# Performance work log

Hardware: AMD Instinct MI355X
Metric: run time of the kernel (lower is better)

The kernel has to match this reference:

```python
import jax, jax.numpy as jnp
import numpy as np

START_TIME = 10
CODING_TIME = 10
REMAIN_TIME = 5
V_TH = 1.0

# surrogate-gradient spike: forward is Heaviside(x>0)
@jax.custom_vjp
def spike(x):
    return (x > 0).astype(x.dtype)

def _spike_fwd(x):
    return spike(x), x

def _spike_bwd(x, g):
    lens = 0.5
    gamma = 0.5
    temp = jnp.exp(-x * x / (2.0 * lens * lens)) / jnp.sqrt(2.0 * jnp.pi) / lens
    return (g * temp * gamma,)

spike.defvjp(_spike_fwd, _spike_bwd)

B, T, I, H, O = 500, 100, 700, 512, 20

def setup_inputs() -> dict:
    key = jax.random.key(0)
    ks = jax.random.split(key, 9)
    half = I // 2
    input_data = jax.random.normal(ks[0], (B, T, I), dtype=jnp.float32)
    target = jax.random.randint(ks[1], (B, T), 0, O, dtype=jnp.int32).astype(jnp.int64)
    v_init = jax.random.uniform(ks[2], (B, H), dtype=jnp.float32)  # torch.rand init
    lim = 1.0 / np.sqrt(half)
    W1 = jax.random.uniform(ks[3], (H, half), minval=-lim, maxval=lim, dtype=jnp.float32)
    W2 = jax.random.uniform(ks[4], (H, half), minval=-lim, maxval=lim, dtype=jnp.float32)
    tau_n = jax.random.uniform(ks[5], (2, H), minval=2.0, maxval=6.0, dtype=jnp.float32)
    tau_m = jax.random.uniform(ks[6], (H,), minval=0.0, maxval=4.0, dtype=jnp.float32)
    lim_o = 1.0 / np.sqrt(H)
    Wout = jax.random.uniform(ks[7], (O, H), minval=-lim_o, maxval=lim_o, dtype=jnp.float32)
    bout = jax.random.uniform(ks[8], (O,), minval=-lim_o, maxval=lim_o, dtype=jnp.float32)
    return {"input_data": input_data, "target": target, "v_init": v_init,
            "W1": W1, "W2": W2, "tau_n": tau_n, "tau_m": tau_m,
            "Wout": Wout, "bout": bout}

def reference(input_data, target, v_init, W1, W2, tau_n, tau_m, Wout, bout):
    Bs, Ts, Is = input_data.shape
    half = Is // 2
    # precompute both branch drives for all timesteps: [T, B, H]
    b1 = jnp.einsum('bti,hi->tbh', input_data[:, :, :half], W1)
    b2 = jnp.einsum('bti,hi->tbh', input_data[:, :, half:], W2)
    beta1 = jax.nn.sigmoid(tau_n[0])  # [H]
    beta2 = jax.nn.sigmoid(tau_n[1])  # [H]
    alpha = jax.nn.sigmoid(tau_m)     # [H]

    def step(carry, inp):
        d1, d2, v, s = carry
        x1, x2 = inp
        d1 = beta1 * d1 + (1.0 - beta1) * x1
        d2 = beta2 * d2 + (1.0 - beta2) * x2
        v = alpha * v + (1.0 - alpha) * (d1 + d2) - V_TH * s
        s = spike(v - V_TH)
        return (d1, d2, v, s), s

    z = jnp.zeros_like(v_init)
    (_, _, _, _), spikes = jax.lax.scan(step, (z, z, v_init, z), (b1, b2))  # spikes: [T,B,H]
    output_history = jnp.einsum('tbh,oh->bto', spikes, Wout) + bout  # [B,T,O]

    ts = np.arange(Ts)
    mask_np = ((ts - START_TIME) % (CODING_TIME + REMAIN_TIME) > REMAIN_TIME) & (ts > START_TIME)
    mask = jnp.asarray(mask_np, dtype=output_history.dtype)  # [T]

    # faithful double-softmax: CrossEntropyLoss applied to softmax(output)
    p = jax.nn.softmax(output_history, axis=-1)
    logp = jax.nn.log_softmax(p, axis=-1)
    tgt = target.astype(jnp.int32)
    ce = -jnp.take_along_axis(logp, tgt[..., None], axis=-1)[..., 0]  # [B,T]
    loss_per_t = ce.mean(axis=0)  # mean over batch, per timestep
    total_loss = jnp.sum(loss_per_t * mask)

    pred = jnp.argmax(p, axis=-1)  # [B,T]
    total_correct = jnp.sum((pred == tgt).astype(jnp.int32) * mask_np[None, :].astype(np.int32))
    total_samples = int(mask_np.sum()) * Bs
    return total_loss, output_history, total_correct, total_samples
```

## Files before the change

kernel.cpp:

```cpp
#include <hip/hip_runtime.h>
#include <hip/hip_bf16.h>
#include <math.h>

#define B_    500
#define T_    100
#define I_    700
#define HALF_ 350
#define H_    512
#define O_    20
#define M_    (B_*T_)
#define BH_   (B_*H_)
#define TP_   112
#define KP_   352
#define ASTR_ 40
#define ABUF_ (TP_*ASTR_)
#define DRB_  116
#define NB_   12500

#define START_T  10
#define CODING_T 10
#define REMAIN_T 5

typedef __attribute__((ext_vector_type(8))) short short8v;
typedef __attribute__((ext_vector_type(8))) unsigned short ushort8v;
typedef __attribute__((ext_vector_type(4))) float f32x4;
typedef __attribute__((ext_vector_type(2))) float f32x2;

__device__ __forceinline__ float sigmoidf_(float x) {
  return 1.0f / (1.0f + expf(-x));
}

__device__ __forceinline__ unsigned cvtpk(float lo, float hi) {
  unsigned r;
  asm("v_cvt_pk_bf16_f32 %0, %1, %2" : "=v"(r) : "v"(lo), "v"(hi));
  return r;
}

__device__ __forceinline__ unsigned cvtpk_fp8x4(float f0, float f1, float f2, float f3) {
  int r = __builtin_amdgcn_cvt_pk_fp8_f32(f0, f1, 0, false);
  r = __builtin_amdgcn_cvt_pk_fp8_f32(f2, f3, r, true);
  return (unsigned)r;
}

__device__ __forceinline__ unsigned short f2bf(float f) {
  unsigned u = __float_as_uint(f);
  u = (u + 0x7fffu + ((u >> 16) & 1u)) >> 16;
  return (unsigned short)u;
}

__global__ __launch_bounds__(256) void convert_w(
    const float* __restrict__ W1, const float* __restrict__ W2,
    unsigned short* __restrict__ wb)
{
  const int idx = blockIdx.x * 256 + threadIdx.x;
  const int ph  = idx / (H_ * (KP_ / 8));
  const int rem = idx % (H_ * (KP_ / 8));
  const int h   = rem / (KP_ / 8);
  const int cc  = (rem % (KP_ / 8)) * 8;
  ushort8v v;
#pragma unroll
  for (int j = 0; j < 8; ++j) {
    const int kk = cc + j;
    float f;
    if (ph == 0) f = (kk < HALF_) ? W1[(size_t)h * HALF_ + kk] : 0.0f;
    else         f = (kk >= 2)    ? W2[(size_t)h * HALF_ + kk - 2] : 0.0f;
    v[j] = f2bf(f);
  }
  *reinterpret_cast<ushort8v*>(wb + (((size_t)ph * H_ + h) * KP_) + cc) = v;
}

__global__ __launch_bounds__(1024, 4) void fused_drive_scan(
    const float* __restrict__ input, const unsigned short* __restrict__ Wb,
    const float* __restrict__ v_init, const float* __restrict__ tau_n,
    const float* __restrict__ tau_m, unsigned char* __restrict__ spikes)
{
  __shared__ __align__(16) unsigned short As[2 * ABUF_];
  __shared__ __align__(4) unsigned char d1c[H_ * DRB_];
  __shared__ __align__(4) unsigned char d2c[H_ * DRB_];

  const int tid  = threadIdx.x;
  const int lane = tid & 63;
  const int w    = tid >> 6;
  const int b    = blockIdx.x;

  const int sr = tid >> 3;
  const int so = (tid & 7) * 4;
  const bool stLd = (tid < 800);
  const bool stZr = (tid >= 800) && (tid < 896);
  const float* aBase = input + ((size_t)b * T_ + (stLd ? sr : 0)) * I_ + so;
  unsigned short* aDst = As + sr * ASTR_ + so;

  const int brow = w * 32 + (lane & 15);
  const int kcS  = (lane >> 4) * 8;
  const unsigned short* bBase0 = Wb + (size_t)brow * KP_ + kcS;
  const unsigned short* bBase1 = Wb + (size_t)(brow + 16) * KP_ + kcS;
  const int arow = lane & 15;

  f32x4 acc[7][2];
#pragma unroll
  for (int i = 0; i < 7; ++i) {
    acc[i][0] = f32x4{0.f, 0.f, 0.f, 0.f};
    acc[i][1] = f32x4{0.f, 0.f, 0.f, 0.f};
  }

  float4 aR;
  short8v bC0, bC1, bN0, bN1;

  if (stZr) {
    const uint2 z = {0, 0};
    *(uint2*)(aDst) = z;
    *(uint2*)(aDst + ABUF_) = z;
  }
  if (stLd) aR = *(const float4*)(aBase);
  bC0 = *reinterpret_cast<const short8v*>(bBase0);
  bC1 = *reinterpret_cast<const short8v*>(bBase1);
  bN0 = *reinterpret_cast<const short8v*>(bBase0 + 32);
  bN1 = *reinterpret_cast<const short8v*>(bBase1 + 32);
  if (stLd) {
    const uint2 p = {cvtpk(aR.x, aR.y), cvtpk(aR.z, aR.w)};
    *(uint2*)(aDst) = p;
    aR = *(const float4*)(aBase + 32);
  }
  asm volatile("s_waitcnt lgkmcnt(0)" ::: "memory");
  __builtin_amdgcn_s_barrier();
  asm volatile("" ::: "memory");

#pragma unroll 1
  for (int k = 0; k < 22; ++k) {
    const int buf  = (k & 1) * ABUF_;
    const int nbuf = ((k + 1) & 1) * ABUF_;
    short8v a[7];
#pragma unroll
    for (int i = 0; i < 7; ++i)
      a[i] = *reinterpret_cast<const short8v*>(As + buf + (arow + i * 16) * ASTR_ + kcS);
#pragma unroll
    for (int i = 0; i < 7; ++i) {
      acc[i][0] = __builtin_amdgcn_mfma_f32_16x16x32_bf16(a[i], bC0, acc[i][0], 0, 0, 0);
      acc[i][1] = __builtin_amdgcn_mfma_f32_16x16x32_bf16(a[i], bC1, acc[i][1], 0, 0, 0);
    }
    bC0 = bN0; bC1 = bN1;
    if (k < 21 && stLd) {
      const uint2 p = {cvtpk(aR.x, aR.y), cvtpk(aR.z, aR.w)};
      *(uint2*)(aDst + nbuf) = p;
    }
    if (k < 20 && stLd) {
      const int kn  = k + 2;
      const int ph  = (kn >= 11);
      const int k0  = (kn - ph * 11) * 32;
      aR = *(const float4*)(aBase + (ph ? 348 : 0) + k0);
    }
    if (k < 20) {
      const int kb  = k + 2;
      const int phb = (kb >= 11);
      const size_t bo = (size_t)phb * H_ * KP_ + (kb - phb * 11) * 32;
      bN0 = *reinterpret_cast<const short8v*>(bBase0 + bo);
      bN1 = *reinterpret_cast<const short8v*>(bBase1 + bo);
    }
    if (k == 10 || k == 21) {
      unsigned char* ds = (k == 10) ? d1c : d2c;
#pragma unroll
      for (int i = 0; i < 7; ++i) {
        const int tb = i * 16 + ((lane >> 4) << 2);
#pragma unroll
        for (int j = 0; j < 2; ++j) {
          const int hl = w * 32 + j * 16 + (lane & 15);
          const unsigned r =
              cvtpk_fp8x4(acc[i][j][0], acc[i][j][1], acc[i][j][2], acc[i][j][3]);
          *(unsigned*)(ds + hl * DRB_ + tb) = r;
          acc[i][j] = f32x4{0.f, 0.f, 0.f, 0.f};
        }
      }
    }
    asm volatile("s_waitcnt lgkmcnt(0)" ::: "memory");
    __builtin_amdgcn_s_barrier();
    asm volatile("" ::: "memory");
  }

  if (tid < H_) {
    const int hg = tid;
    const float beta1 = sigmoidf_(tau_n[hg]);
    const float beta2 = sigmoidf_(tau_n[H_ + hg]);
    const float alpha = sigmoidf_(tau_m[hg]);
    const float ob1 = 1.0f - beta1, ob2 = 1.0f - beta2, oa = 1.0f - alpha;

    float d1 = 0.0f, d2 = 0.0f, s = 0.0f;
    float v = v_init[(size_t)b * H_ + hg];
    const unsigned char* r1 = d1c + hg * DRB_;
    const unsigned char* r2 = d2c + hg * DRB_;
    unsigned char* sp = spikes + (size_t)b * (T_ * H_) + hg;
#pragma unroll 1
    for (int c = 0; c < 25; ++c) {
      const unsigned u1 = *(const unsigned*)(r1 + c * 4);
      const unsigned u2 = *(const unsigned*)(r2 + c * 4);
      const f32x2 a1 = __builtin_amdgcn_cvt_pk_f32_fp8((int)u1, false);
      const f32x2 b1 = __builtin_amdgcn_cvt_pk_f32_fp8((int)u1, true);
      const f32x2 a2 = __builtin_amdgcn_cvt_pk_f32_fp8((int)u2, false);
      const f32x2 b2 = __builtin_amdgcn_cvt_pk_f32_fp8((int)u2, true);
      const float f1[4] = {a1[0], a1[1], b1[0], b1[1]};
      const float f2[4] = {a2[0], a2[1], b2[0], b2[1]};
#pragma unroll
      for (int j = 0; j < 4; ++j) {
        d1 = beta1 * d1 + ob1 * f1[j];
        d2 = beta2 * d2 + ob2 * f2[j];
        v = alpha * v + oa * (d1 + d2) - s;
        s = (v > 1.0f) ? 1.0f : 0.0f;
        sp[(size_t)(c * 4 + j) * H_] = (unsigned char)s;
      }
    }
  }
}

__global__ __launch_bounds__(256) void out_loss(
    const unsigned char* __restrict__ spikes, const float* __restrict__ Wout,
    const float* __restrict__ bout, const int* __restrict__ target,
    float* __restrict__ oh, float* __restrict__ partials)
{
  const int lane = threadIdx.x & 63;
  const int widx = threadIdx.x >> 6;
  const int bt = blockIdx.x * 4 + widx;
  const int t = bt % T_;

  const uint2 sv = *(const uint2*)(spikes + (size_t)bt * H_ + lane * 8);

  float acc[O_];
#pragma unroll
  for (int o = 0; o < O_; ++o) acc[o] = 0.0f;

#pragma unroll
  for (int j = 0; j < 8; ++j) {
    const unsigned sb = ((j < 4) ? (sv.x >> (8 * j)) : (sv.y >> (8 * (j - 4)))) & 255u;
    if (sb) {
      const int hh = lane * 8 + j;
#pragma unroll
      for (int o = 0; o < O_; ++o) acc[o] += Wout[o * H_ + hh];
    }
  }
#pragma unroll
  for (int o = 0; o < O_; ++o) {
#pragma unroll
    for (int off = 32; off; off >>= 1) acc[o] += __shfl_xor(acc[o], off);
    acc[o] += bout[o];
  }
  if (lane < O_) oh[(size_t)bt * O_ + lane] = acc[lane];

  __shared__ float sl[4], sc[4];
  float lossc = 0.0f, corr = 0.0f;
  const bool maskv = (t > START_T) && (((t - START_T) % (CODING_T + REMAIN_T)) > REMAIN_T);
  if (maskv) {
    const int tgt = target[bt];
    float m = acc[0];
    int pred = 0;
#pragma unroll
    for (int o = 1; o < O_; ++o) { if (acc[o] > m) { m = acc[o]; pred = o; } }
    float S = 0.0f, etgt = 0.0f;
#pragma unroll
    for (int o = 0; o < O_; ++o) {
      const float eo = expf(acc[o] - m);
      S += eo;
      if (o == tgt) etgt = eo;
    }
    const float inv = 1.0f / S;
    float S2 = 0.0f;
#pragma unroll
    for (int o = 0; o < O_; ++o) S2 += expf(expf(acc[o] - m) * inv - inv);
    lossc = (inv + logf(S2) - etgt * inv) * (1.0f / (float)B_);
    corr = (pred == tgt) ? 1.0f : 0.0f;
  }
  if (lane == 0) { sl[widx] = lossc; sc[widx] = corr; }
  __syncthreads();
  if (threadIdx.x == 0) {
    partials[blockIdx.x]       = sl[0] + sl[1] + sl[2] + sl[3];
    partials[NB_ + blockIdx.x] = sc[0] + sc[1] + sc[2] + sc[3];
  }
}

__global__ __launch_bounds__(256) void loss_final(
    const float* __restrict__ partials, float* __restrict__ out, float samples)
{
  float a = 0.0f, c = 0.0f;
  for (int i = threadIdx.x; i < NB_; i += 256) { a += partials[i]; c += partials[NB_ + i]; }
  __shared__ float sl[256], sc[256];
  sl[threadIdx.x] = a; sc[threadIdx.x] = c;
  __syncthreads();
  for (int s = 128; s > 0; s >>= 1) {
    if (threadIdx.x < s) {
      sl[threadIdx.x] += sl[threadIdx.x + s];
      sc[threadIdx.x] += sc[threadIdx.x + s];
    }
    __syncthreads();
  }
  if (threadIdx.x == 0) {
    out[0] = sl[0];
    out[1 + (size_t)M_ * O_] = sc[0];
    out[2 + (size_t)M_ * O_] = samples;
  }
}

extern "C" void kernel_launch(void* const* d_in, const int* in_sizes, int n_in,
                              void* d_out, int out_size, void* d_ws, size_t ws_size,
                              hipStream_t stream) {
  const float* input  = (const float*)d_in[0];
  const int*   target = (const int*)d_in[1];
  const float* v_init = (const float*)d_in[2];
  const float* W1     = (const float*)d_in[3];
  const float* W2     = (const float*)d_in[4];
  const float* tau_n  = (const float*)d_in[5];
  const float* tau_m  = (const float*)d_in[6];
  const float* Wout   = (const float*)d_in[7];
  const float* bout   = (const float*)d_in[8];
  float* out = (float*)d_out;
  float* oh  = out + 1;

  unsigned short* Wb = (unsigned short*)d_ws;
  unsigned char* spikes = (unsigned char*)(Wb + (size_t)2 * H_ * KP_);
  float* partials = (float*)(spikes + (size_t)B_ * T_ * H_);

  hipLaunchKernelGGL(convert_w, dim3((2 * H_ * KP_ / 8) / 256), dim3(256), 0, stream,
                     W1, W2, Wb);

  hipLaunchKernelGGL(fused_drive_scan, dim3(B_), dim3(1024), 0, stream,
                     input, Wb, v_init, tau_n, tau_m, spikes);

  hipLaunchKernelGGL(out_loss, dim3(NB_), dim3(256), 0, stream,
                     spikes, Wout, bout, target, oh, partials);

  int mcount = 0;
  for (int t = 0; t < T_; ++t)
    if (t > START_T && ((t - START_T) % (CODING_T + REMAIN_T)) > REMAIN_T) mcount++;
  hipLaunchKernelGGL(loss_final, dim3(1), dim3(256), 0, stream, partials,
                     out, (float)(mcount * B_));
}
```

Before: 162.6 us.

## Split fused drive-scan across two blocks per batch row by hidden half

Each batch element's drive GEMM and scan is now handled by two 512-thread blocks, each covering 256 hidden units, instead of one 1024-thread block covering all 512. This doubles the grid to 1000 blocks and halves the per-block LDS used for the fp8 drive buffers, which should let more blocks share a CU and improve occupancy and load balance. The A-tile staging is widened so each thread converts 8 floats per step. The cost is that each batch row's input slice is loaded and converted twice, once per hidden half.

```diff
diff --git a/kernel.cpp b/kernel.cpp
--- a/kernel.cpp
+++ b/kernel.cpp
@@ -14,6 +14,7 @@
 #define KP_   352
 #define ASTR_ 40
 #define ABUF_ (TP_*ASTR_)
+#define HH_   256
 #define DRB_  116
 #define NB_   12500
 
@@ -69,28 +70,31 @@
   *reinterpret_cast<ushort8v*>(wb + (((size_t)ph * H_ + h) * KP_) + cc) = v;
 }
 
-__global__ __launch_bounds__(1024, 4) void fused_drive_scan(
+__global__ __launch_bounds__(512, 4) void fused_drive_scan(
     const float* __restrict__ input, const unsigned short* __restrict__ Wb,
     const float* __restrict__ v_init, const float* __restrict__ tau_n,
     const float* __restrict__ tau_m, unsigned char* __restrict__ spikes)
 {
   __shared__ __align__(16) unsigned short As[2 * ABUF_];
-  __shared__ __align__(4) unsigned char d1c[H_ * DRB_];
-  __shared__ __align__(4) unsigned char d2c[H_ * DRB_];
+  __shared__ __align__(4) unsigned char d1c[HH_ * DRB_];
+  __shared__ __align__(4) unsigned char d2c[HH_ * DRB_];
 
   const int tid  = threadIdx.x;
   const int lane = tid & 63;
   const int w    = tid >> 6;
-  const int b    = blockIdx.x;
-
-  const int sr = tid >> 3;
-  const int so = (tid & 7) * 4;
-  const bool stLd = (tid < 800);
-  const bool stZr = (tid >= 800) && (tid < 896);
-  const float* aBase = input + ((size_t)b * T_ + (stLd ? sr : 0)) * I_ + so;
-  unsigned short* aDst = As + sr * ASTR_ + so;
-
-  const int brow = w * 32 + (lane & 15);
+  const int id   = blockIdx.x;
+  const int b    = id >> 1;
+  const int hh   = id & 1;
+  const int h0g  = hh * HH_;
+
+  const int sr = tid >> 2;
+  const int sc = (tid & 3) * 8;
+  const bool stLd = (sr < T_);
+  const bool stZr = (sr >= T_) && (sr < TP_);
+  const float* aBase = input + ((size_t)b * T_ + (stLd ? sr : 0)) * I_ + sc;
+  unsigned short* aDst = As + sr * ASTR_ + sc;
+
+  const int brow = h0g + w * 32 + (lane & 15);
   const int kcS  = (lane >> 4) * 8;
   const unsigned short* bBase0 = Wb + (size_t)brow * KP_ + kcS;
   const unsigned short* bBase1 = Wb + (size_t)(brow + 16) * KP_ + kcS;
@@ -103,23 +107,28 @@
     acc[i][1] = f32x4{0.f, 0.f, 0.f, 0.f};
   }
 
-  float4 aR;
+  float4 aR0, aR1;
   short8v bC0, bC1, bN0, bN1;
 
   if (stZr) {
-    const uint2 z = {0, 0};
-    *(uint2*)(aDst) = z;
-    *(uint2*)(aDst + ABUF_) = z;
-  }
-  if (stLd) aR = *(const float4*)(aBase);
+    const uint4 z = {0, 0, 0, 0};
+    *(uint4*)(aDst) = z;
+    *(uint4*)(aDst + ABUF_) = z;
+  }
+  if (stLd) {
+    aR0 = *(const float4*)(aBase);
+    aR1 = *(const float4*)(aBase + 4);
+  }
   bC0 = *reinterpret_cast<const short8v*>(bBase0);
   bC1 = *reinterpret_cast<const short8v*>(bBase1);
   bN0 = *reinterpret_cast<const short8v*>(bBase0 + 32);
   bN1 = *reinterpret_cast<const short8v*>(bBase1 + 32);
   if (stLd) {
-    const uint2 p = {cvtpk(aR.x, aR.y), cvtpk(aR.z, aR.w)};
-    *(uint2*)(aDst) = p;
-    aR = *(const float4*)(aBase + 32);
+    const uint4 p = {cvtpk(aR0.x, aR0.y), cvtpk(aR0.z, aR0.w),
+                     cvtpk(aR1.x, aR1.y), cvtpk(aR1.z, aR1.w)};
+    *(uint4*)(aDst) = p;
+    aR0 = *(const float4*)(aBase + 32);
+    aR1 = *(const float4*)(aBase + 36);
   }
   asm volatile("s_waitcnt lgkmcnt(0)" ::: "memory");
   __builtin_amdgcn_s_barrier();
@@ -140,14 +149,17 @@
     }
     bC0 = bN0; bC1 = bN1;
     if (k < 21 && stLd) {
-      const uint2 p = {cvtpk(aR.x, aR.y), cvtpk(aR.z, aR.w)};
-      *(uint2*)(aDst + nbuf) = p;
+      const uint4 p = {cvtpk(aR0.x, aR0.y), cvtpk(aR0.z, aR0.w),
+                       cvtpk(aR1.x, aR1.y), cvtpk(aR1.z, aR1.w)};
+      *(uint4*)(aDst + nbuf) = p;
     }
     if (k < 20 && stLd) {
       const int kn  = k + 2;
       const int ph  = (kn >= 11);
       const int k0  = (kn - ph * 11) * 32;
-      aR = *(const float4*)(aBase + (ph ? 348 : 0) + k0);
+      const float* ap = aBase + (ph ? 348 : 0) + k0;
+      aR0 = *(const float4*)(ap);
+      aR1 = *(const float4*)(ap + 4);
     }
     if (k < 20) {
       const int kb  = k + 2;
@@ -176,8 +188,8 @@
     asm volatile("" ::: "memory");
   }
 
-  if (tid < H_) {
-    const int hg = tid;
+  if (tid < HH_) {
+    const int hg = h0g + tid;
     const float beta1 = sigmoidf_(tau_n[hg]);
     const float beta2 = sigmoidf_(tau_n[H_ + hg]);
     const float alpha = sigmoidf_(tau_m[hg]);
@@ -185,8 +197,8 @@
 
     float d1 = 0.0f, d2 = 0.0f, s = 0.0f;
     float v = v_init[(size_t)b * H_ + hg];
-    const unsigned char* r1 = d1c + hg * DRB_;
-    const unsigned char* r2 = d2c + hg * DRB_;
+    const unsigned char* r1 = d1c + tid * DRB_;
+    const unsigned char* r2 = d2c + tid * DRB_;
     unsigned char* sp = spikes + (size_t)b * (T_ * H_) + hg;
 #pragma unroll 1
     for (int c = 0; c < 25; ++c) {
@@ -318,7 +330,7 @@
   hipLaunchKernelGGL(convert_w, dim3((2 * H_ * KP_ / 8) / 256), dim3(256), 0, stream,
                      W1, W2, Wb);
 
-  hipLaunchKernelGGL(fused_drive_scan, dim3(B_), dim3(1024), 0, stream,
+  hipLaunchKernelGGL(fused_drive_scan, dim3(2 * B_), dim3(512), 0, stream,
                      input, Wb, v_init, tau_n, tau_m, spikes);
 
   hipLaunchKernelGGL(out_loss, dim3(NB_), dim3(256), 0, stream,
```

Measured after the change: 165.1 us. No clear change (+1.5%).

## Load input tiles directly into LDS as fp32 and convert to bf16 on fragment read

Applied to the files above, without the earlier changes.

Input rows now go straight from global memory into a double-buffered fp32 LDS tile through global_load_lds, replacing the old path of staging in registers, converting, and storing bf16 into LDS. Each wave converts fp32 to bf16 when it reads its MFMA A fragments, and the loop syncs on vmcnt instead of lgkmcnt. The aim is to drop the register staging step and its latency from the GEMM prologue and loop. In exchange, LDS read traffic doubles and every wave repeats the same conversion work. Padded rows past T now load row 0 data instead of zeros.

```diff
diff --git a/kernel.cpp b/kernel.cpp
--- a/kernel.cpp
+++ b/kernel.cpp
@@ -12,8 +12,7 @@
 #define BH_   (B_*H_)
 #define TP_   112
 #define KP_   352
-#define ASTR_ 40
-#define ABUF_ (TP_*ASTR_)
+#define AFP_  3584
 #define DRB_  116
 #define NB_   12500
 
@@ -46,6 +45,12 @@
   unsigned u = __float_as_uint(f);
   u = (u + 0x7fffu + ((u >> 16) & 1u)) >> 16;
   return (unsigned short)u;
+}
+
+__device__ __forceinline__ void gload16f(const float* g, float* l) {
+  __builtin_amdgcn_global_load_lds(
+      (const __attribute__((address_space(1))) unsigned int*)g,
+      (__attribute__((address_space(3))) unsigned int*)l, 16, 0, 0);
 }
 
 __global__ __launch_bounds__(256) void convert_w(
@@ -74,7 +79,7 @@
     const float* __restrict__ v_init, const float* __restrict__ tau_n,
     const float* __restrict__ tau_m, unsigned char* __restrict__ spikes)
 {
-  __shared__ __align__(16) unsigned short As[2 * ABUF_];
+  __shared__ __align__(16) float Af[2 * AFP_];
   __shared__ __align__(4) unsigned char d1c[H_ * DRB_];
   __shared__ __align__(4) unsigned char d2c[H_ * DRB_];
 
@@ -83,18 +88,18 @@
   const int w    = tid >> 6;
   const int b    = blockIdx.x;
 
-  const int sr = tid >> 3;
-  const int so = (tid & 7) * 4;
-  const bool stLd = (tid < 800);
-  const bool stZr = (tid >= 800) && (tid < 896);
-  const float* aBase = input + ((size_t)b * T_ + (stLd ? sr : 0)) * I_ + so;
-  unsigned short* aDst = As + sr * ASTR_ + so;
+  const int srow = tid >> 3;
+  const int trow = (srow < T_) ? srow : 0;
+  const bool stOn = (tid < 896);
+  const float* aRow = input + ((size_t)b * T_ + trow) * I_ + (tid & 7) * 4;
+  float* aDst = Af + tid * 4;
 
   const int brow = w * 32 + (lane & 15);
   const int kcS  = (lane >> 4) * 8;
   const unsigned short* bBase0 = Wb + (size_t)brow * KP_ + kcS;
   const unsigned short* bBase1 = Wb + (size_t)(brow + 16) * KP_ + kcS;
   const int arow = lane & 15;
+  const int kcF  = (lane >> 4) * 8;
 
   f32x4 acc[7][2];
 #pragma unroll
@@ -103,52 +108,46 @@
     acc[i][1] = f32x4{0.f, 0.f, 0.f, 0.f};
   }
 
-  float4 aR;
   short8v bC0, bC1, bN0, bN1;
 
-  if (stZr) {
-    const uint2 z = {0, 0};
-    *(uint2*)(aDst) = z;
-    *(uint2*)(aDst + ABUF_) = z;
-  }
-  if (stLd) aR = *(const float4*)(aBase);
+  if (stOn) gload16f(aRow, aDst);
+  asm volatile("" ::: "memory");
   bC0 = *reinterpret_cast<const short8v*>(bBase0);
   bC1 = *reinterpret_cast<const short8v*>(bBase1);
+  asm volatile("" ::: "memory");
   bN0 = *reinterpret_cast<const short8v*>(bBase0 + 32);
   bN1 = *reinterpret_cast<const short8v*>(bBase1 + 32);
-  if (stLd) {
-    const uint2 p = {cvtpk(aR.x, aR.y), cvtpk(aR.z, aR.w)};
-    *(uint2*)(aDst) = p;
-    aR = *(const float4*)(aBase + 32);
-  }
-  asm volatile("s_waitcnt lgkmcnt(0)" ::: "memory");
+  asm volatile("s_waitcnt vmcnt(2)" ::: "memory");
   __builtin_amdgcn_s_barrier();
   asm volatile("" ::: "memory");
 
 #pragma unroll 1
   for (int k = 0; k < 22; ++k) {
-    const int buf  = (k & 1) * ABUF_;
-    const int nbuf = ((k + 1) & 1) * ABUF_;
+    const int buf  = (k & 1) * AFP_;
+    const int nbuf = ((k + 1) & 1) * AFP_;
     short8v a[7];
 #pragma unroll
-    for (int i = 0; i < 7; ++i)
-      a[i] = *reinterpret_cast<const short8v*>(As + buf + (arow + i * 16) * ASTR_ + kcS);
+    for (int i = 0; i < 7; ++i) {
+      const float* fp = Af + buf + (arow + i * 16) * 32 + kcF;
+      const f32x4 lo = *reinterpret_cast<const f32x4*>(fp);
+      const f32x4 hi = *reinterpret_cast<const f32x4*>(fp + 4);
+      uint4 u = {cvtpk(lo[0], lo[1]), cvtpk(lo[2], lo[3]),
+                 cvtpk(hi[0], hi[1]), cvtpk(hi[2], hi[3])};
+      a[i] = *reinterpret_cast<short8v*>(&u);
+    }
 #pragma unroll
     for (int i = 0; i < 7; ++i) {
       acc[i][0] = __builtin_amdgcn_mfma_f32_16x16x32_bf16(a[i], bC0, acc[i][0], 0, 0, 0);
       acc[i][1] = __builtin_amdgcn_mfma_f32_16x16x32_bf16(a[i], bC1, acc[i][1], 0, 0, 0);
     }
     bC0 = bN0; bC1 = bN1;
-    if (k < 21 && stLd) {
-      const uint2 p = {cvtpk(aR.x, aR.y), cvtpk(aR.z, aR.w)};
-      *(uint2*)(aDst + nbuf) = p;
-    }
-    if (k < 20 && stLd) {
-      const int kn  = k + 2;
-      const int ph  = (kn >= 11);
-      const int k0  = (kn - ph * 11) * 32;
-      aR = *(const float4*)(aBase + (ph ? 348 : 0) + k0);
-    }
+    if (k < 21 && stOn) {
+      const int kn = k + 1;
+      const int ph = (kn >= 11);
+      const int k0 = (kn - ph * 11) * 32;
+      gload16f(aRow + (ph ? 348 : 0) + k0, Af + nbuf + tid * 4);
+    }
+    asm volatile("" ::: "memory");
     if (k < 20) {
       const int kb  = k + 2;
       const int phb = (kb >= 11);
@@ -170,8 +169,10 @@
           acc[i][j] = f32x4{0.f, 0.f, 0.f, 0.f};
         }
       }
-    }
-    asm volatile("s_waitcnt lgkmcnt(0)" ::: "memory");
+      asm volatile("s_waitcnt lgkmcnt(0)" ::: "memory");
+    }
+    if (k >= 20) asm volatile("s_waitcnt vmcnt(0)" ::: "memory");
+    else         asm volatile("s_waitcnt vmcnt(2)" ::: "memory");
     __builtin_amdgcn_s_barrier();
     asm volatile("" ::: "memory");
   }
```

Measured after the change: 202.2 us. +24.4%, slower.
